# Kernel tuning notes

Hardware: AMD Instinct MI355X
Metric: run time of the kernel (lower is better)

Reference implementation:

```python
import jax, jax.numpy as jnp
import numpy as np

B = 4096          # players (batch)
DEG = 64          # asteroids per player
A = B * DEG       # total asteroids
E = A             # one edge per asteroid (asteroid -> its player)
PD, AD, ED = 5, 3, 7
HID = 64
HEADS = 4
OUT = HID         # GATv2Conv out_channels (concat=False -> mean over heads)
L = 2             # num_layers
NEG_SLOPE = 0.2
LN_EPS = 1e-5


def setup_inputs() -> dict:
    key = jax.random.key(0)
    ks = jax.random.split(key, 20)
    f = jnp.float32
    inp = {}
    inp["player_feat"] = jax.random.normal(ks[0], (B, PD), f)
    inp["asteroid_feat"] = jax.random.normal(ks[1], (A, AD), f)
    src = jnp.arange(E, dtype=jnp.int32)
    dst = src // DEG                      # player batch index per edge
    inp["edge_index"] = jnp.stack([src, dst])  # [2, E] int32
    inp["edge_attr"] = jax.random.normal(ks[2], (E, ED), f)
    sc = 0.1
    # input projections
    inp["Wp"] = jax.random.normal(ks[3], (PD, HID), f) * sc
    inp["bp"] = jnp.zeros((HID,), f)
    inp["Wa"] = jax.random.normal(ks[4], (AD, HID), f) * sc
    inp["ba"] = jnp.zeros((HID,), f)
    # per-layer GATv2 params (stacked over L)
    inp["Wl"] = jax.random.normal(ks[5], (L, HID, HEADS * OUT), f) * sc
    inp["bl"] = jnp.zeros((L, HEADS * OUT), f)
    inp["Wr"] = jax.random.normal(ks[6], (L, HID, HEADS * OUT), f) * sc
    inp["br"] = jnp.zeros((L, HEADS * OUT), f)
    inp["We"] = jax.random.normal(ks[7], (L, ED, HEADS * OUT), f) * sc
    inp["att"] = jax.random.normal(ks[8], (L, HEADS, OUT), f) * sc
    inp["bias"] = jnp.zeros((L, OUT), f)
    inp["ln_g"] = jnp.ones((L, HID), f)
    inp["ln_b"] = jnp.zeros((L, HID), f)
    return inp


def _layer_norm(x, g, b):
    mu = jnp.mean(x, axis=-1, keepdims=True)
    var = jnp.mean(jnp.square(x - mu), axis=-1, keepdims=True)
    return (x - mu) * jax.lax.rsqrt(var + LN_EPS) * g + b


def _gatv2(x, src, dst, edge_attr, Wl, bl, Wr, br, We, att, bias, n_nodes):
    # x: [N, HID]; src/dst: [E]; PyG GATv2Conv, add_self_loops=False, concat=False
    xl = (x @ Wl + bl).reshape(-1, HEADS, OUT)   # source transform
    xr = (x @ Wr + br).reshape(-1, HEADS, OUT)   # target transform
    ea = (edge_attr @ We).reshape(-1, HEADS, OUT)
    e = xl[src] + xr[dst] + ea                   # [E, H, O]
    e = jnp.where(e >= 0, e, NEG_SLOPE * e)      # LeakyReLU(0.2)
    logits = jnp.einsum('eho,ho->eh', e, att)    # [E, H]
    # segment softmax over incoming edges of each target node
    m = jax.ops.segment_max(logits, dst, num_segments=n_nodes)
    al = jnp.exp(logits - m[dst])
    den = jax.ops.segment_sum(al, dst, num_segments=n_nodes)
    alpha = al / den[dst]                        # [E, H]
    msg = alpha[:, :, None] * xl[src]            # [E, H, O]
    out = jax.ops.segment_sum(msg, dst, num_segments=n_nodes)  # [N, H, O]
    return jnp.mean(out, axis=1) + bias          # concat=False -> head mean


def reference(player_feat, asteroid_feat, edge_index, edge_attr,
              Wp, bp, Wa, ba, Wl, bl, Wr, br, We, att, bias, ln_g, ln_b):
    batch = player_feat.shape[0]
    h_p = jax.nn.relu(player_feat @ Wp + bp)
    h_a = jax.nn.relu(asteroid_feat @ Wa + ba)
    x = jnp.concatenate([h_p, h_a], axis=0)      # [N, HID]
    n_nodes = x.shape[0]
    src = edge_index[0] + batch                  # asteroid local -> global idx
    dst = edge_index[1]
    for i in range(L):
        x_new = _gatv2(x, src, dst, edge_attr, Wl[i], bl[i], Wr[i], br[i],
                       We[i], att[i], bias[i], n_nodes)
        x = _layer_norm(x + jax.nn.relu(x_new), ln_g[i], ln_b[i])
    return x[:batch]
```

## Files before the change

kernel.cpp:

```cpp
#include <hip/hip_runtime.h>


typedef __bf16 bf16x8 __attribute__((ext_vector_type(8)));
typedef float  f32x4  __attribute__((ext_vector_type(4)));

union FragU { unsigned short u[8]; bf16x8 v; };

__device__ __forceinline__ float bf2f(unsigned short u) {
    union { unsigned int i; float f; } v; v.i = ((unsigned int)u) << 16; return v.f;
}
__device__ __forceinline__ unsigned short f2bf(float f) {
    union { __bf16 b; unsigned short u; } x; x.b = (__bf16)f; return x.u;
}

#define NEG_SLOPE 0.2f
#define LN_EPS 1e-5f
#define XS 88
#define LPS 17

struct Smem {
    __align__(16) unsigned short xa[64 * XS];
    __align__(16) unsigned short xpb[64];
    float lpb[4 * 64 * LPS];
    float alf[256];
    float outp[256];
    float xp[64];
    float afs[192];
    float rbs[64], gs[64], bs[64];
    float sbl[256], satt[256], sbr[256];
};

__global__ __launch_bounds__(256) void prep_weights(
    const float* __restrict__ Wl, const float* __restrict__ Wr,
    const float* __restrict__ We,
    unsigned short* __restrict__ wlf, unsigned short* __restrict__ wrf,
    unsigned short* __restrict__ wef)
{
    int i = blockIdx.x * 256 + threadIdx.x;
    int jj = i & 7, t = (i >> 3) & 255, frag = (i >> 11) & 7, layer = (i >> 14) & 1;
    int nt = frag >> 1, ko = frag & 1;
    int c = (t >> 6) * 64 + nt * 16 + (t & 15);
    int kb = ko * 32 + ((t >> 4) & 3) * 8;
    wlf[i] = f2bf(Wl[layer * 16384 + (kb + jj) * 256 + c]);
    wrf[i] = f2bf(Wr[layer * 16384 + (kb + jj) * 256 + c]);
    if (i < 16384) {
        int j2 = i & 7, t2 = (i >> 3) & 255, n2 = (i >> 11) & 3, l2 = (i >> 13) & 1;
        int q2 = (t2 >> 4) & 3;
        int c2 = (t2 >> 6) * 64 + n2 * 16 + (t2 & 15);
        wef[i] = (q2 == 0 && j2 < 7) ? f2bf(We[l2 * 1792 + j2 * 256 + c2])
                                     : (unsigned short)0;
    }
}

template <bool WS>
__global__ __launch_bounds__(256) void gnn_main(
    const float* __restrict__ pf, const float* __restrict__ af,
    const float* __restrict__ eat, const float* __restrict__ Wp,
    const float* __restrict__ bp, const float* __restrict__ Wa,
    const float* __restrict__ ba, const float* __restrict__ Wl,
    const float* __restrict__ bl, const float* __restrict__ Wr,
    const float* __restrict__ br, const float* __restrict__ We,
    const float* __restrict__ att, const float* __restrict__ bias,
    const float* __restrict__ lng, const float* __restrict__ lnb,
    const unsigned short* __restrict__ wlf, const unsigned short* __restrict__ wrf,
    const unsigned short* __restrict__ wef, float* __restrict__ out)
{
    __shared__ Smem sm;
    const int p = blockIdx.x, t = threadIdx.x;
    const int w = t >> 6, l = t & 63, q = l >> 4, m = l & 15;
    const int cbase = w * 64;

    if (t < 192) sm.afs[t] = af[p * 192 + t];
    if (t < 64) {
        sm.rbs[t] = fmaxf(bias[t], 0.f);
        sm.gs[t] = lng[t];
        sm.bs[t] = lnb[t];
        float acc = bp[t];
        #pragma unroll
        for (int d = 0; d < 5; ++d) acc += pf[p * 5 + d] * Wp[d * 64 + t];
        float xp0 = fmaxf(acc, 0.f);
        sm.xp[t] = xp0;
        sm.xpb[t] = f2bf(xp0);
    }
    __syncthreads();
    {
        const int k = t & 63;
        float wa0 = Wa[k], wa1 = Wa[64 + k], wa2 = Wa[128 + k], bak = ba[k];
        #pragma unroll
        for (int rep = 0; rep < 16; ++rep) {
            int j = rep * 4 + (t >> 6);
            float acc = bak + sm.afs[j * 3] * wa0 + sm.afs[j * 3 + 1] * wa1
                      + sm.afs[j * 3 + 2] * wa2;
            sm.xa[j * XS + k] = f2bf(fmaxf(acc, 0.f));
        }
    }
    #pragma unroll
    for (int idx = t; idx < 512; idx += 256) {
        int j = idx >> 3, d = idx & 7;
        sm.xa[j * XS + 64 + d] = (d < 7) ? f2bf(eat[(p * 64 + j) * 7 + d])
                                         : (unsigned short)0;
    }

    f32x4 accT[16];

    for (int layer = 0; layer < 2; ++layer) {
        sm.sbl[t]  = bl[layer * 256 + t];
        sm.satt[t] = att[layer * 256 + t];
        sm.sbr[t]  = br[layer * 256 + t];
        __syncthreads();

        float xrc[4];
        {
            FragU xf0, xf1;
            xf0.v = *reinterpret_cast<const bf16x8*>(&sm.xpb[q * 8]);
            xf1.v = *reinterpret_cast<const bf16x8*>(&sm.xpb[32 + q * 8]);
            #pragma unroll
            for (int nt = 0; nt < 4; ++nt) {
                int c = cbase + nt * 16 + m;
                FragU r0, r1;
                if constexpr (WS) {
                    r0.v = *reinterpret_cast<const bf16x8*>(&wrf[((layer * 8 + nt * 2 + 0) * 256 + t) * 8]);
                    r1.v = *reinterpret_cast<const bf16x8*>(&wrf[((layer * 8 + nt * 2 + 1) * 256 + t) * 8]);
                } else {
                    #pragma unroll
                    for (int jj = 0; jj < 8; ++jj) {
                        r0.u[jj] = f2bf(Wr[layer * 16384 + (q * 8 + jj) * 256 + c]);
                        r1.u[jj] = f2bf(Wr[layer * 16384 + (32 + q * 8 + jj) * 256 + c]);
                    }
                }
                float sb = sm.sbr[c];
                f32x4 cx = { sb, sb, sb, sb };
                cx = __builtin_amdgcn_mfma_f32_16x16x32_bf16(xf0.v, r0.v, cx, 0, 0, 0);
                cx = __builtin_amdgcn_mfma_f32_16x16x32_bf16(xf1.v, r1.v, cx, 0, 0, 0);
                xrc[nt] = cx[0];
            }
        }

        FragU bfr[8];
        bf16x8 ebf[4];
        if constexpr (WS) {
            #pragma unroll
            for (int f = 0; f < 8; ++f)
                bfr[f].v = *reinterpret_cast<const bf16x8*>(&wlf[((layer * 8 + f) * 256 + t) * 8]);
            #pragma unroll
            for (int nt = 0; nt < 4; ++nt)
                ebf[nt] = *reinterpret_cast<const bf16x8*>(&wef[((layer * 4 + nt) * 256 + t) * 8]);
        } else {
            const float* Wli = Wl + layer * 16384;
            #pragma unroll
            for (int nt = 0; nt < 4; ++nt) {
                int c = cbase + nt * 16 + m;
                #pragma unroll
                for (int ko = 0; ko < 2; ++ko) {
                    int kb = ko * 32 + q * 8;
                    #pragma unroll
                    for (int jj = 0; jj < 8; ++jj)
                        bfr[nt * 2 + ko].u[jj] = f2bf(Wli[(kb + jj) * 256 + c]);
                }
                FragU e;
                #pragma unroll
                for (int jj = 0; jj < 8; ++jj)
                    e.u[jj] = (q == 0 && jj < 7) ? f2bf(We[layer * 1792 + jj * 256 + c])
                                                 : (unsigned short)0;
                ebf[nt] = e.v;
            }
        }
        float blc[4], aoc[4];
        #pragma unroll
        for (int nt = 0; nt < 4; ++nt) {
            int c = cbase + nt * 16 + m;
            blc[nt] = sm.sbl[c];
            aoc[nt] = sm.satt[c];
        }

        float lp[16];
        #pragma unroll
        for (int i = 0; i < 16; ++i) lp[i] = 0.f;

        #pragma unroll
        for (int mt = 0; mt < 4; ++mt) {
            const int row = mt * 16 + m;
            bf16x8 a0 = *reinterpret_cast<const bf16x8*>(&sm.xa[row * XS + q * 8]);
            bf16x8 a1 = *reinterpret_cast<const bf16x8*>(&sm.xa[row * XS + 32 + q * 8]);
            bf16x8 a2 = *reinterpret_cast<const bf16x8*>(&sm.xa[row * XS + 64]);
            #pragma unroll
            for (int nt = 0; nt < 4; ++nt) {
                f32x4 c1 = { blc[nt], blc[nt], blc[nt], blc[nt] };
                c1 = __builtin_amdgcn_mfma_f32_16x16x32_bf16(a0, bfr[nt * 2 + 0].v, c1, 0, 0, 0);
                c1 = __builtin_amdgcn_mfma_f32_16x16x32_bf16(a1, bfr[nt * 2 + 1].v, c1, 0, 0, 0);
                accT[mt * 4 + nt] = c1;
                f32x4 c2 = { xrc[nt], xrc[nt], xrc[nt], xrc[nt] };
                c2 = __builtin_amdgcn_mfma_f32_16x16x32_bf16(a2, ebf[nt], c2, 0, 0, 0);
                #pragma unroll
                for (int r = 0; r < 4; ++r) {
                    float ev = c1[r] + c2[r];
                    ev = fmaxf(ev, NEG_SLOPE * ev);
                    lp[mt * 4 + r] += ev * aoc[nt];
                }
            }
        }

        {
            float* lpw = &sm.lpb[w * 64 * LPS];
            #pragma unroll
            for (int mt = 0; mt < 4; ++mt)
                #pragma unroll
                for (int r = 0; r < 4; ++r)
                    lpw[(mt * 16 + q * 4 + r) * LPS + m] = lp[mt * 4 + r];
        }
        __syncthreads();
        {
            const float* lpw = &sm.lpb[w * 64 * LPS];
            float lg = 0.f;
            #pragma unroll
            for (int mm = 0; mm < 16; ++mm) lg += lpw[l * LPS + mm];
            float mx = lg;
            #pragma unroll
            for (int msk = 1; msk <= 32; msk <<= 1) mx = fmaxf(mx, __shfl_xor(mx, msk, 64));
            float al = __expf(lg - mx);
            float den = al;
            #pragma unroll
            for (int msk = 1; msk <= 32; msk <<= 1) den += __shfl_xor(den, msk, 64);
            sm.alf[w * 64 + l] = al / den;
        }
        __syncthreads();

        {
            const float* alw = &sm.alf[w * 64];
            float al16[16];
            #pragma unroll
            for (int mt = 0; mt < 4; ++mt)
                #pragma unroll
                for (int r = 0; r < 4; ++r)
                    al16[mt * 4 + r] = alw[mt * 16 + q * 4 + r];
            #pragma unroll
            for (int nt = 0; nt < 4; ++nt) {
                float s = 0.f;
                #pragma unroll
                for (int i = 0; i < 16; ++i) s += al16[i] * accT[(i >> 2) * 4 + nt][i & 3];
                s += __shfl_xor(s, 16, 64);
                s += __shfl_xor(s, 32, 64);
                if (q == 0) sm.outp[cbase + nt * 16 + m] = s;
            }
        }
        __syncthreads();

        if (layer == 0) {
            const int j = t >> 2, part = t & 3;
            unsigned short* rowp = &sm.xa[j * XS + part * 16];
            FragU A0, A1;
            A0.v = *reinterpret_cast<const bf16x8*>(rowp);
            A1.v = *reinterpret_cast<const bf16x8*>(rowp + 8);
            float v[16], sum = 0.f, sq = 0.f;
            #pragma unroll
            for (int i = 0; i < 16; ++i) {
                unsigned short us = (i < 8) ? A0.u[i] : A1.u[i - 8];
                float x = bf2f(us) + sm.rbs[part * 16 + i];
                v[i] = x; sum += x; sq += x * x;
            }
            sum += __shfl_xor(sum, 1, 64); sq += __shfl_xor(sq, 1, 64);
            sum += __shfl_xor(sum, 2, 64); sq += __shfl_xor(sq, 2, 64);
            float mu = sum * (1.f / 64.f);
            float var = sq * (1.f / 64.f) - mu * mu;
            float rs = rsqrtf(var + LN_EPS);
            FragU O0, O1;
            #pragma unroll
            for (int i = 0; i < 16; ++i) {
                int col = part * 16 + i;
                unsigned short ub = f2bf((v[i] - mu) * rs * sm.gs[col] + sm.bs[col]);
                if (i < 8) O0.u[i] = ub; else O1.u[i - 8] = ub;
            }
            *reinterpret_cast<bf16x8*>(rowp) = O0.v;
            *reinterpret_cast<bf16x8*>(rowp + 8) = O1.v;
        }
        if (t < 64) {
            float xnew = 0.25f * (sm.outp[t] + sm.outp[64 + t] + sm.outp[128 + t] + sm.outp[192 + t])
                       + bias[layer * 64 + t];
            float v = sm.xp[t] + fmaxf(xnew, 0.f);
            float sum = v, sq = v * v;
            #pragma unroll
            for (int msk = 1; msk <= 32; msk <<= 1) {
                sum += __shfl_xor(sum, msk, 64);
                sq  += __shfl_xor(sq,  msk, 64);
            }
            float mu = sum * (1.f / 64.f);
            float var = sq * (1.f / 64.f) - mu * mu;
            float y = (v - mu) * rsqrtf(var + LN_EPS) * lng[layer * 64 + t]
                    + lnb[layer * 64 + t];
            sm.xp[t] = y;
            sm.xpb[t] = f2bf(y);
        }
        __syncthreads();
    }

    if (t < 64) out[p * 64 + t] = sm.xp[t];
}

extern "C" void kernel_launch(void* const* d_in, const int* in_sizes, int n_in,
                              void* d_out, int out_size, void* d_ws, size_t ws_size,
                              hipStream_t stream) {
    const float* pf   = (const float*)d_in[0];
    const float* af   = (const float*)d_in[1];
    const float* eat  = (const float*)d_in[3];
    const float* Wp   = (const float*)d_in[4];
    const float* bp   = (const float*)d_in[5];
    const float* Wa   = (const float*)d_in[6];
    const float* ba   = (const float*)d_in[7];
    const float* Wl   = (const float*)d_in[8];
    const float* bl   = (const float*)d_in[9];
    const float* Wr   = (const float*)d_in[10];
    const float* br   = (const float*)d_in[11];
    const float* We   = (const float*)d_in[12];
    const float* att  = (const float*)d_in[13];
    const float* bias = (const float*)d_in[14];
    const float* lng  = (const float*)d_in[15];
    const float* lnb  = (const float*)d_in[16];
    float* out = (float*)d_out;

    const int B = in_sizes[0] / 5;
    unsigned short* wlf = (unsigned short*)d_ws;
    unsigned short* wrf = wlf + 32768;
    unsigned short* wef = wrf + 32768;
    const size_t need = (32768 + 32768 + 16384) * sizeof(unsigned short);

    if (ws_size >= need) {
        prep_weights<<<dim3(128), dim3(256), 0, stream>>>(Wl, Wr, We, wlf, wrf, wef);
        gnn_main<true><<<dim3(B), dim3(256), 0, stream>>>(
            pf, af, eat, Wp, bp, Wa, ba, Wl, bl, Wr, br, We, att, bias, lng, lnb,
            wlf, wrf, wef, out);
    } else {
        gnn_main<false><<<dim3(B), dim3(256), 0, stream>>>(
            pf, af, eat, Wp, bp, Wa, ba, Wl, bl, Wr, br, We, att, bias, lng, lnb,
            wlf, wrf, wef, out);
    }
}
```

Before: 181.7 us.

## Do softmax reductions in registers via shuffles and preload bias vectors from workspace

Replaces the shared-memory logit buffer and alpha array with in-register butterfly shuffles: the 16-lane column sum, max and denominator are reduced across lanes, and the unnormalized exponentials are applied directly to the accumulators. This removes two block-wide barriers and a large LDS staging area per layer. The bias and attention vectors are prepacked into per-thread float4 layouts by the prep kernel, so the per-layer LDS stores and barrier disappear. The final layer also skips the unneeded asteroid LayerNorm and writes the output directly. The cost is extra shuffle instructions and extra workspace.

```diff
diff --git a/kernel.cpp b/kernel.cpp
--- a/kernel.cpp
+++ b/kernel.cpp
@@ -16,25 +16,25 @@
 #define NEG_SLOPE 0.2f
 #define LN_EPS 1e-5f
 #define XS 88
-#define LPS 17
 
 struct Smem {
     __align__(16) unsigned short xa[64 * XS];
     __align__(16) unsigned short xpb[64];
-    float lpb[4 * 64 * LPS];
-    float alf[256];
     float outp[256];
     float xp[64];
     float afs[192];
     float rbs[64], gs[64], bs[64];
-    float sbl[256], satt[256], sbr[256];
 };
+
+#define WS_NEED (163840 + 3 * 8192)
 
 __global__ __launch_bounds__(256) void prep_weights(
     const float* __restrict__ Wl, const float* __restrict__ Wr,
-    const float* __restrict__ We,
+    const float* __restrict__ We, const float* __restrict__ bl,
+    const float* __restrict__ att, const float* __restrict__ br,
     unsigned short* __restrict__ wlf, unsigned short* __restrict__ wrf,
-    unsigned short* __restrict__ wef)
+    unsigned short* __restrict__ wef, f32x4* __restrict__ blq,
+    f32x4* __restrict__ attq, f32x4* __restrict__ brq)
 {
     int i = blockIdx.x * 256 + threadIdx.x;
     int jj = i & 7, t = (i >> 3) & 255, frag = (i >> 11) & 7, layer = (i >> 14) & 1;
@@ -50,6 +50,19 @@
         wef[i] = (q2 == 0 && j2 < 7) ? f2bf(We[l2 * 1792 + j2 * 256 + c2])
                                      : (unsigned short)0;
     }
+    if (i < 512) {
+        int lyr = i >> 8, tt = i & 255;
+        int hb = (tt >> 6) * 64, mm = tt & 15;
+        f32x4 b, a, r;
+        #pragma unroll
+        for (int n = 0; n < 4; ++n) {
+            int cc = hb + n * 16 + mm;
+            b[n] = bl[lyr * 256 + cc];
+            a[n] = att[lyr * 256 + cc];
+            r[n] = br[lyr * 256 + cc];
+        }
+        blq[i] = b; attq[i] = a; brq[i] = r;
+    }
 }
 
 template <bool WS>
@@ -63,7 +76,9 @@
     const float* __restrict__ att, const float* __restrict__ bias,
     const float* __restrict__ lng, const float* __restrict__ lnb,
     const unsigned short* __restrict__ wlf, const unsigned short* __restrict__ wrf,
-    const unsigned short* __restrict__ wef, float* __restrict__ out)
+    const unsigned short* __restrict__ wef, const f32x4* __restrict__ blq,
+    const f32x4* __restrict__ attq, const f32x4* __restrict__ brq,
+    float* __restrict__ out)
 {
     __shared__ Smem sm;
     const int p = blockIdx.x, t = threadIdx.x;
@@ -100,14 +115,25 @@
         sm.xa[j * XS + 64 + d] = (d < 7) ? f2bf(eat[(p * 64 + j) * 7 + d])
                                          : (unsigned short)0;
     }
+    __syncthreads();
 
     f32x4 accT[16];
 
     for (int layer = 0; layer < 2; ++layer) {
-        sm.sbl[t]  = bl[layer * 256 + t];
-        sm.satt[t] = att[layer * 256 + t];
-        sm.sbr[t]  = br[layer * 256 + t];
-        __syncthreads();
+        f32x4 blv, atv, brv;
+        if constexpr (WS) {
+            blv = blq[layer * 256 + t];
+            atv = attq[layer * 256 + t];
+            brv = brq[layer * 256 + t];
+        } else {
+            #pragma unroll
+            for (int nt = 0; nt < 4; ++nt) {
+                int c = cbase + nt * 16 + m;
+                blv[nt] = bl[layer * 256 + c];
+                atv[nt] = att[layer * 256 + c];
+                brv[nt] = br[layer * 256 + c];
+            }
+        }
 
         float xrc[4];
         {
@@ -116,20 +142,19 @@
             xf1.v = *reinterpret_cast<const bf16x8*>(&sm.xpb[32 + q * 8]);
             #pragma unroll
             for (int nt = 0; nt < 4; ++nt) {
-                int c = cbase + nt * 16 + m;
                 FragU r0, r1;
                 if constexpr (WS) {
                     r0.v = *reinterpret_cast<const bf16x8*>(&wrf[((layer * 8 + nt * 2 + 0) * 256 + t) * 8]);
                     r1.v = *reinterpret_cast<const bf16x8*>(&wrf[((layer * 8 + nt * 2 + 1) * 256 + t) * 8]);
                 } else {
+                    int c = cbase + nt * 16 + m;
                     #pragma unroll
                     for (int jj = 0; jj < 8; ++jj) {
                         r0.u[jj] = f2bf(Wr[layer * 16384 + (q * 8 + jj) * 256 + c]);
                         r1.u[jj] = f2bf(Wr[layer * 16384 + (32 + q * 8 + jj) * 256 + c]);
                     }
                 }
-                float sb = sm.sbr[c];
-                f32x4 cx = { sb, sb, sb, sb };
+                f32x4 cx = { brv[nt], brv[nt], brv[nt], brv[nt] };
                 cx = __builtin_amdgcn_mfma_f32_16x16x32_bf16(xf0.v, r0.v, cx, 0, 0, 0);
                 cx = __builtin_amdgcn_mfma_f32_16x16x32_bf16(xf1.v, r1.v, cx, 0, 0, 0);
                 xrc[nt] = cx[0];
@@ -165,13 +190,6 @@
                 ebf[nt] = e.v;
             }
         }
-        float blc[4], aoc[4];
-        #pragma unroll
-        for (int nt = 0; nt < 4; ++nt) {
-            int c = cbase + nt * 16 + m;
-            blc[nt] = sm.sbl[c];
-            aoc[nt] = sm.satt[c];
-        }
 
         float lp[16];
         #pragma unroll
@@ -185,7 +203,7 @@
             bf16x8 a2 = *reinterpret_cast<const bf16x8*>(&sm.xa[row * XS + 64]);
             #pragma unroll
             for (int nt = 0; nt < 4; ++nt) {
-                f32x4 c1 = { blc[nt], blc[nt], blc[nt], blc[nt] };
+                f32x4 c1 = { blv[nt], blv[nt], blv[nt], blv[nt] };
                 c1 = __builtin_amdgcn_mfma_f32_16x16x32_bf16(a0, bfr[nt * 2 + 0].v, c1, 0, 0, 0);
                 c1 = __builtin_amdgcn_mfma_f32_16x16x32_bf16(a1, bfr[nt * 2 + 1].v, c1, 0, 0, 0);
                 accT[mt * 4 + nt] = c1;
@@ -195,105 +213,108 @@
                 for (int r = 0; r < 4; ++r) {
                     float ev = c1[r] + c2[r];
                     ev = fmaxf(ev, NEG_SLOPE * ev);
-                    lp[mt * 4 + r] += ev * aoc[nt];
-                }
-            }
-        }
-
-        {
-            float* lpw = &sm.lpb[w * 64 * LPS];
-            #pragma unroll
-            for (int mt = 0; mt < 4; ++mt)
-                #pragma unroll
-                for (int r = 0; r < 4; ++r)
-                    lpw[(mt * 16 + q * 4 + r) * LPS + m] = lp[mt * 4 + r];
+                    lp[mt * 4 + r] += ev * atv[nt];
+                }
+            }
+        }
+
+        #pragma unroll
+        for (int i = 0; i < 16; ++i) {
+            float v = lp[i];
+            v += __shfl_xor(v, 1, 64);
+            v += __shfl_xor(v, 2, 64);
+            v += __shfl_xor(v, 4, 64);
+            v += __shfl_xor(v, 8, 64);
+            lp[i] = v;
+        }
+        float mx = lp[0];
+        #pragma unroll
+        for (int i = 1; i < 16; ++i) mx = fmaxf(mx, lp[i]);
+        mx = fmaxf(mx, __shfl_xor(mx, 16, 64));
+        mx = fmaxf(mx, __shfl_xor(mx, 32, 64));
+        float den = 0.f;
+        #pragma unroll
+        for (int i = 0; i < 16; ++i) { lp[i] = __expf(lp[i] - mx); den += lp[i]; }
+        den += __shfl_xor(den, 16, 64);
+        den += __shfl_xor(den, 32, 64);
+        const float rden = 1.f / den;
+
+        #pragma unroll
+        for (int nt = 0; nt < 4; ++nt) {
+            float s = 0.f;
+            #pragma unroll
+            for (int i = 0; i < 16; ++i) s += lp[i] * accT[(i >> 2) * 4 + nt][i & 3];
+            s *= rden;
+            s += __shfl_xor(s, 16, 64);
+            s += __shfl_xor(s, 32, 64);
+            if (q == 0) sm.outp[cbase + nt * 16 + m] = s;
         }
         __syncthreads();
-        {
-            const float* lpw = &sm.lpb[w * 64 * LPS];
-            float lg = 0.f;
-            #pragma unroll
-            for (int mm = 0; mm < 16; ++mm) lg += lpw[l * LPS + mm];
-            float mx = lg;
-            #pragma unroll
-            for (int msk = 1; msk <= 32; msk <<= 1) mx = fmaxf(mx, __shfl_xor(mx, msk, 64));
-            float al = __expf(lg - mx);
-            float den = al;
-            #pragma unroll
-            for (int msk = 1; msk <= 32; msk <<= 1) den += __shfl_xor(den, msk, 64);
-            sm.alf[w * 64 + l] = al / den;
-        }
-        __syncthreads();
-
-        {
-            const float* alw = &sm.alf[w * 64];
-            float al16[16];
-            #pragma unroll
-            for (int mt = 0; mt < 4; ++mt)
-                #pragma unroll
-                for (int r = 0; r < 4; ++r)
-                    al16[mt * 4 + r] = alw[mt * 16 + q * 4 + r];
-            #pragma unroll
-            for (int nt = 0; nt < 4; ++nt) {
-                float s = 0.f;
-                #pragma unroll
-                for (int i = 0; i < 16; ++i) s += al16[i] * accT[(i >> 2) * 4 + nt][i & 3];
-                s += __shfl_xor(s, 16, 64);
-                s += __shfl_xor(s, 32, 64);
-                if (q == 0) sm.outp[cbase + nt * 16 + m] = s;
-            }
-        }
-        __syncthreads();
 
         if (layer == 0) {
-            const int j = t >> 2, part = t & 3;
-            unsigned short* rowp = &sm.xa[j * XS + part * 16];
-            FragU A0, A1;
-            A0.v = *reinterpret_cast<const bf16x8*>(rowp);
-            A1.v = *reinterpret_cast<const bf16x8*>(rowp + 8);
-            float v[16], sum = 0.f, sq = 0.f;
-            #pragma unroll
-            for (int i = 0; i < 16; ++i) {
-                unsigned short us = (i < 8) ? A0.u[i] : A1.u[i - 8];
-                float x = bf2f(us) + sm.rbs[part * 16 + i];
-                v[i] = x; sum += x; sq += x * x;
-            }
-            sum += __shfl_xor(sum, 1, 64); sq += __shfl_xor(sq, 1, 64);
-            sum += __shfl_xor(sum, 2, 64); sq += __shfl_xor(sq, 2, 64);
-            float mu = sum * (1.f / 64.f);
-            float var = sq * (1.f / 64.f) - mu * mu;
-            float rs = rsqrtf(var + LN_EPS);
-            FragU O0, O1;
-            #pragma unroll
-            for (int i = 0; i < 16; ++i) {
-                int col = part * 16 + i;
-                unsigned short ub = f2bf((v[i] - mu) * rs * sm.gs[col] + sm.bs[col]);
-                if (i < 8) O0.u[i] = ub; else O1.u[i - 8] = ub;
-            }
-            *reinterpret_cast<bf16x8*>(rowp) = O0.v;
-            *reinterpret_cast<bf16x8*>(rowp + 8) = O1.v;
-        }
-        if (t < 64) {
-            float xnew = 0.25f * (sm.outp[t] + sm.outp[64 + t] + sm.outp[128 + t] + sm.outp[192 + t])
-                       + bias[layer * 64 + t];
-            float v = sm.xp[t] + fmaxf(xnew, 0.f);
-            float sum = v, sq = v * v;
-            #pragma unroll
-            for (int msk = 1; msk <= 32; msk <<= 1) {
-                sum += __shfl_xor(sum, msk, 64);
-                sq  += __shfl_xor(sq,  msk, 64);
-            }
-            float mu = sum * (1.f / 64.f);
-            float var = sq * (1.f / 64.f) - mu * mu;
-            float y = (v - mu) * rsqrtf(var + LN_EPS) * lng[layer * 64 + t]
-                    + lnb[layer * 64 + t];
-            sm.xp[t] = y;
-            sm.xpb[t] = f2bf(y);
-        }
-        __syncthreads();
-    }
-
-    if (t < 64) out[p * 64 + t] = sm.xp[t];
+            {
+                const int j = t >> 2, part = t & 3;
+                unsigned short* rowp = &sm.xa[j * XS + part * 16];
+                FragU A0, A1;
+                A0.v = *reinterpret_cast<const bf16x8*>(rowp);
+                A1.v = *reinterpret_cast<const bf16x8*>(rowp + 8);
+                float v[16], sum = 0.f, sq = 0.f;
+                #pragma unroll
+                for (int i = 0; i < 16; ++i) {
+                    unsigned short us = (i < 8) ? A0.u[i] : A1.u[i - 8];
+                    float x = bf2f(us) + sm.rbs[part * 16 + i];
+                    v[i] = x; sum += x; sq += x * x;
+                }
+                sum += __shfl_xor(sum, 1, 64); sq += __shfl_xor(sq, 1, 64);
+                sum += __shfl_xor(sum, 2, 64); sq += __shfl_xor(sq, 2, 64);
+                float mu = sum * (1.f / 64.f);
+                float var = sq * (1.f / 64.f) - mu * mu;
+                float rs = rsqrtf(var + LN_EPS);
+                FragU O0, O1;
+                #pragma unroll
+                for (int i = 0; i < 16; ++i) {
+                    int col = part * 16 + i;
+                    unsigned short ub = f2bf((v[i] - mu) * rs * sm.gs[col] + sm.bs[col]);
+                    if (i < 8) O0.u[i] = ub; else O1.u[i - 8] = ub;
+                }
+                *reinterpret_cast<bf16x8*>(rowp) = O0.v;
+                *reinterpret_cast<bf16x8*>(rowp + 8) = O1.v;
+            }
+            if (t < 64) {
+                float xnew = 0.25f * (sm.outp[t] + sm.outp[64 + t] + sm.outp[128 + t] + sm.outp[192 + t])
+                           + bias[t];
+                float v = sm.xp[t] + fmaxf(xnew, 0.f);
+                float sum = v, sq = v * v;
+                #pragma unroll
+                for (int msk = 1; msk <= 32; msk <<= 1) {
+                    sum += __shfl_xor(sum, msk, 64);
+                    sq  += __shfl_xor(sq,  msk, 64);
+                }
+                float mu = sum * (1.f / 64.f);
+                float var = sq * (1.f / 64.f) - mu * mu;
+                float y = (v - mu) * rsqrtf(var + LN_EPS) * lng[t] + lnb[t];
+                sm.xp[t] = y;
+                sm.xpb[t] = f2bf(y);
+            }
+            __syncthreads();
+        } else {
+            if (t < 64) {
+                float xnew = 0.25f * (sm.outp[t] + sm.outp[64 + t] + sm.outp[128 + t] + sm.outp[192 + t])
+                           + bias[64 + t];
+                float v = sm.xp[t] + fmaxf(xnew, 0.f);
+                float sum = v, sq = v * v;
+                #pragma unroll
+                for (int msk = 1; msk <= 32; msk <<= 1) {
+                    sum += __shfl_xor(sum, msk, 64);
+                    sq  += __shfl_xor(sq,  msk, 64);
+                }
+                float mu = sum * (1.f / 64.f);
+                float var = sq * (1.f / 64.f) - mu * mu;
+                float y = (v - mu) * rsqrtf(var + LN_EPS) * lng[64 + t] + lnb[64 + t];
+                out[p * 64 + t] = y;
+            }
+        }
+    }
 }
 
 extern "C" void kernel_launch(void* const* d_in, const int* in_sizes, int n_in,
@@ -321,16 +342,19 @@
     unsigned short* wlf = (unsigned short*)d_ws;
     unsigned short* wrf = wlf + 32768;
     unsigned short* wef = wrf + 32768;
-    const size_t need = (32768 + 32768 + 16384) * sizeof(unsigned short);
-
-    if (ws_size >= need) {
-        prep_weights<<<dim3(128), dim3(256), 0, stream>>>(Wl, Wr, We, wlf, wrf, wef);
+    f32x4* blq  = (f32x4*)((char*)d_ws + 163840);
+    f32x4* attq = blq + 512;
+    f32x4* brq  = attq + 512;
+
+    if (ws_size >= WS_NEED) {
+        prep_weights<<<dim3(128), dim3(256), 0, stream>>>(
+            Wl, Wr, We, bl, att, br, wlf, wrf, wef, blq, attq, brq);
         gnn_main<true><<<dim3(B), dim3(256), 0, stream>>>(
             pf, af, eat, Wp, bp, Wa, ba, Wl, bl, Wr, br, We, att, bias, lng, lnb,
-            wlf, wrf, wef, out);
+            wlf, wrf, wef, blq, attq, brq, out);
     } else {
         gnn_main<false><<<dim3(B), dim3(256), 0, stream>>>(
             pf, af, eat, Wp, bp, Wa, ba, Wl, bl, Wr, br, We, att, bias, lng, lnb,
-            wlf, wrf, wef, out);
-    }
-}
+            wlf, wrf, wef, blq, attq, brq, out);
+    }
+}
```

New measurement: 187.4 us. +3.2%, slower.
